# Performance work log

Measured on AMD Instinct MI355X. Metric: run time of the kernel, lower is better.

The kernel has to match this reference:

```python
import jax, jax.numpy as jnp
import numpy as np

N_NODES = 100000


def _degrees(src, dst, n):
    ones = jnp.ones(src.shape[0], dtype=jnp.float32)
    deg_out = jax.ops.segment_sum(ones, src, num_segments=n)
    deg_in = jax.ops.segment_sum(ones, dst, num_segments=n)
    # DGL clamps degrees to min 1 before pow(-0.5)
    return jnp.clip(deg_out, 1.0) ** -0.5, jnp.clip(deg_in, 1.0) ** -0.5


def _graph_conv(x, src, dst, W, b, norm_out, norm_in, n):
    # norm='both': scale source by D_out^-1/2, aggregate (copy_u + sum), scale dest by D_in^-1/2
    # weight applied before aggregation (in_feats >= out_feats for all layers; math-equivalent)
    h = (x * norm_out[:, None]) @ W                      # [N, out]
    agg = jax.ops.segment_sum(h[src], dst, num_segments=n)  # SpMM via gather+scatter-add
    return agg * norm_in[:, None] + b


def setup_inputs() -> dict:
    key = jax.random.key(0)
    ks = jax.random.split(key, 8)
    E = 1600000
    return {
        "in_feat": jax.random.normal(ks[0], (N_NODES, 128), dtype=jnp.float32),
        "src": jax.random.randint(ks[1], (E,), 0, N_NODES),
        "dst": jax.random.randint(ks[2], (E,), 0, N_NODES),
        "W1": jax.random.normal(ks[3], (128, 128), dtype=jnp.float32) * (128 ** -0.5),
        "b1": jnp.zeros((128,), dtype=jnp.float32),
        "W2": jax.random.normal(ks[4], (128, 128), dtype=jnp.float32) * (128 ** -0.5),
        "b2": jnp.zeros((128,), dtype=jnp.float32),
        "W3": jax.random.normal(ks[5], (128, 64), dtype=jnp.float32) * (128 ** -0.5),
        "b3": jnp.zeros((64,), dtype=jnp.float32),
    }


def reference(in_feat, src, dst, W1, b1, W2, b2, W3, b3):
    n = in_feat.shape[0]
    norm_out, norm_in = _degrees(src, dst, n)
    h = jax.nn.relu(_graph_conv(in_feat, src, dst, W1, b1, norm_out, norm_in, n))
    h = jax.nn.relu(_graph_conv(h, src, dst, W2, b2, norm_out, norm_in, n))
    h = _graph_conv(h, src, dst, W3, b3, norm_out, norm_in, n)
    return h
```

## Files before the change

kernel.cpp:

```cpp
#include <hip/hip_runtime.h>

#define THREADS 256
#define SCAN_BLK 1024
#define NR 8
#define NC 32
#define RSTRIDE 12544

typedef __attribute__((ext_vector_type(8))) _Float16 half8;
typedef __attribute__((ext_vector_type(4))) float floatx4;

__device__ __forceinline__ ushort f2h(float f) {
    union { _Float16 h; ushort s; } v;
    v.h = (_Float16)f;
    return v.s;
}
__device__ __forceinline__ float h_lo(uint u) {
    union { ushort s; _Float16 h; } v; v.s = (ushort)(u & 0xFFFFu); return (float)v.h;
}
__device__ __forceinline__ float h_hi(uint u) {
    union { ushort s; _Float16 h; } v; v.s = (ushort)(u >> 16); return (float)v.h;
}

__global__ __launch_bounds__(256) void hist_out_kernel(const int* __restrict__ src,
                                                       int* __restrict__ cnt_out,
                                                       int n, int E) {
    __shared__ uint cnt[RSTRIDE];
    const int range = blockIdx.x % NR;
    const int chunk = blockIdx.x / NR;
    const int Rsz = (n + NR - 1) / NR;
    const int lo  = range * Rsz;
    const int R   = min(n - lo, Rsz);
    if (R <= 0) return;
    for (int i = threadIdx.x; i < R; i += THREADS) cnt[i] = 0;
    __syncthreads();
    const int per = (E + NC - 1) / NC;
    const int c0 = chunk * per;
    const int c1 = min(E, c0 + per);
    int i = c0 + threadIdx.x * 4;
    for (; i + 4 <= c1; i += THREADS * 4) {
        int4 v = *(const int4*)(src + i);
        if ((unsigned)(v.x - lo) < (unsigned)R) atomicAdd(&cnt[v.x - lo], 1u);
        if ((unsigned)(v.y - lo) < (unsigned)R) atomicAdd(&cnt[v.y - lo], 1u);
        if ((unsigned)(v.z - lo) < (unsigned)R) atomicAdd(&cnt[v.z - lo], 1u);
        if ((unsigned)(v.w - lo) < (unsigned)R) atomicAdd(&cnt[v.w - lo], 1u);
    }
    if (i < c1) {
        for (int e = i; e < c1 && e < i + 4; ++e) {
            int s = src[e];
            if ((unsigned)(s - lo) < (unsigned)R) atomicAdd(&cnt[s - lo], 1u);
        }
    }
    __syncthreads();
    for (int k = threadIdx.x; k < R; k += THREADS) {
        uint c = cnt[k];
        if (c) atomicAdd(&cnt_out[lo + k], (int)c);
    }
}

__global__ __launch_bounds__(256) void csr_phaseA(const int* __restrict__ dst,
                                                  ushort* __restrict__ PC, int n, int E) {
    __shared__ uint cnt[RSTRIDE / 2];
    const int range = blockIdx.x % NR;
    const int chunk = blockIdx.x / NR;
    const int Rsz = (n + NR - 1) / NR;
    const int lo  = range * Rsz;
    const int R   = min(n - lo, Rsz);
    if (R <= 0) return;
    const int Rp = (R + 2) >> 1;
    for (int i = threadIdx.x; i < Rp; i += THREADS) cnt[i] = 0;
    __syncthreads();
    const int per = (E + NC - 1) / NC;
    const int c0 = chunk * per;
    const int c1 = min(E, c0 + per);
    int i = c0 + threadIdx.x * 4;
    for (; i + 4 <= c1; i += THREADS * 4) {
        int4 v = *(const int4*)(dst + i);
        int kx = v.x - lo, ky = v.y - lo, kz = v.z - lo, kw = v.w - lo;
        if ((unsigned)kx < (unsigned)R) atomicAdd(&cnt[kx >> 1], (kx & 1) ? 65536u : 1u);
        if ((unsigned)ky < (unsigned)R) atomicAdd(&cnt[ky >> 1], (ky & 1) ? 65536u : 1u);
        if ((unsigned)kz < (unsigned)R) atomicAdd(&cnt[kz >> 1], (kz & 1) ? 65536u : 1u);
        if ((unsigned)kw < (unsigned)R) atomicAdd(&cnt[kw >> 1], (kw & 1) ? 65536u : 1u);
    }
    if (i < c1) {
        for (int e = i; e < c1 && e < i + 4; ++e) {
            int k = dst[e] - lo;
            if ((unsigned)k < (unsigned)R) atomicAdd(&cnt[k >> 1], (k & 1) ? 65536u : 1u);
        }
    }
    __syncthreads();
    ushort* pc = PC + (size_t)(range * NC + chunk) * RSTRIDE;
    for (int k = threadIdx.x; k < R; k += THREADS) {
        uint c = cnt[k >> 1];
        pc[k] = (ushort)((k & 1) ? (c >> 16) : (c & 0xFFFFu));
    }
}

__global__ void csr_colsum(const ushort* __restrict__ PC, int* __restrict__ cnt_in, int n) {
    int gk = blockIdx.x * blockDim.x + threadIdx.x;
    if (gk >= n) return;
    const int Rsz = (n + NR - 1) / NR;
    int r = gk / Rsz, k = gk - r * Rsz;
    int t = 0;
    #pragma unroll 4
    for (int c = 0; c < NC; ++c)
        t += PC[(size_t)(r * NC + c) * RSTRIDE + k];
    cnt_in[gk] = t;
}

__global__ void csr_mkbase(const ushort* __restrict__ PC, const int* __restrict__ row_off,
                           int* __restrict__ B, int n) {
    int gk = blockIdx.x * blockDim.x + threadIdx.x;
    if (gk >= n) return;
    const int Rsz = (n + NR - 1) / NR;
    int r = gk / Rsz, k = gk - r * Rsz;
    int base = row_off[gk];
    for (int c = 0; c < NC; ++c) {
        size_t idx = (size_t)(r * NC + c) * RSTRIDE + k;
        B[idx] = base;
        base += PC[idx];
    }
}

__global__ __launch_bounds__(256) void csr_phaseC(const int* __restrict__ src,
                                                  const int* __restrict__ dst,
                                                  const int* __restrict__ B,
                                                  int* __restrict__ csr_src, int n, int E) {
    __shared__ int cur[RSTRIDE];
    const int range = blockIdx.x % NR;
    const int chunk = blockIdx.x / NR;
    const int Rsz = (n + NR - 1) / NR;
    const int lo  = range * Rsz;
    const int R   = min(n - lo, Rsz);
    if (R <= 0) return;
    const int* b = B + (size_t)(range * NC + chunk) * RSTRIDE;
    for (int i = threadIdx.x; i < R; i += THREADS) cur[i] = b[i];
    __syncthreads();
    const int per = (E + NC - 1) / NC;
    const int c0 = chunk * per;
    const int c1 = min(E, c0 + per);
    int i = c0 + threadIdx.x * 4;
    for (; i + 4 <= c1; i += THREADS * 4) {
        int4 d = *(const int4*)(dst + i);
        int4 s = *(const int4*)(src + i);
        int kx = d.x - lo, ky = d.y - lo, kz = d.z - lo, kw = d.w - lo;
        if ((unsigned)kx < (unsigned)R) csr_src[atomicAdd(&cur[kx], 1)] = s.x;
        if ((unsigned)ky < (unsigned)R) csr_src[atomicAdd(&cur[ky], 1)] = s.y;
        if ((unsigned)kz < (unsigned)R) csr_src[atomicAdd(&cur[kz], 1)] = s.z;
        if ((unsigned)kw < (unsigned)R) csr_src[atomicAdd(&cur[kw], 1)] = s.w;
    }
    if (i < c1) {
        for (int e = i; e < c1 && e < i + 4; ++e) {
            int k = dst[e] - lo;
            if ((unsigned)k < (unsigned)R) csr_src[atomicAdd(&cur[k], 1)] = src[e];
        }
    }
}

__global__ void scan_phase1(const int* __restrict__ cnt, int* __restrict__ blk_sums, int n) {
    int base = blockIdx.x * SCAN_BLK;
    int t = threadIdx.x;
    int sum = 0;
    for (int i = t; i < SCAN_BLK; i += THREADS) {
        int idx = base + i;
        sum += (idx < n) ? cnt[idx] : 0;
    }
    __shared__ int wsum[4];
    for (int off = 32; off > 0; off >>= 1) sum += __shfl_down(sum, off);
    if ((t & 63) == 0) wsum[t >> 6] = sum;
    __syncthreads();
    if (t == 0) blk_sums[blockIdx.x] = wsum[0] + wsum[1] + wsum[2] + wsum[3];
}

__global__ void scan_phase2(int* __restrict__ blk_sums, int nb) {
    __shared__ int s[1024];
    int t = threadIdx.x;
    s[t] = (t < nb) ? blk_sums[t] : 0;
    __syncthreads();
    for (int off = 1; off < 1024; off <<= 1) {
        int v = s[t];
        if (t >= off) v += s[t - off];
        __syncthreads();
        s[t] = v;
        __syncthreads();
    }
    if (t < nb) blk_sums[t] = (t == 0) ? 0 : s[t - 1];
}

__global__ void scan_phase3(const int* __restrict__ cnt, const int* __restrict__ cnt_out,
                            const int* __restrict__ blk_sums,
                            int* __restrict__ row_off, float* __restrict__ norm_in,
                            float* __restrict__ norm_out, int n, int E) {
    __shared__ int ts[THREADS];
    int b = blockIdx.x, t = threadIdx.x;
    int base = b * SCAN_BLK + t * 4;
    int local[4], val[4]; int s = 0;
    #pragma unroll
    for (int k = 0; k < 4; ++k) {
        local[k] = s;
        int idx = base + k;
        int v = (idx < n) ? cnt[idx] : 0;
        val[k] = v;
        s += v;
    }
    ts[t] = s;
    __syncthreads();
    for (int off = 1; off < THREADS; off <<= 1) {
        int v = ts[t];
        if (t >= off) v += ts[t - off];
        __syncthreads();
        ts[t] = v;
        __syncthreads();
    }
    int excl = (t == 0) ? 0 : ts[t - 1];
    int boff = blk_sums[b];
    #pragma unroll
    for (int k = 0; k < 4; ++k) {
        int idx = base + k;
        if (idx < n) {
            row_off[idx] = boff + excl + local[k];
            norm_in[idx]  = rsqrtf((float)max(val[k], 1));
            norm_out[idx] = rsqrtf((float)max(cnt_out[idx], 1));
        }
    }
    if (b == 0 && t == 0) row_off[n] = E;
}

__device__ __forceinline__ void wpack_one(const float* __restrict__ W, ushort* __restrict__ Wpk,
                                          int OUT, int t) {
    int lane = t & 63, kk = (t >> 6) & 3, ct = t >> 8;
    int col = ct * 16 + (lane & 15);
    int k0 = kk * 32 + (lane >> 4) * 8;
    #pragma unroll
    for (int j = 0; j < 8; ++j)
        Wpk[t * 8 + j] = f2h(W[(size_t)(k0 + j) * OUT + col]);
}

__global__ void wpack_all(const float* __restrict__ W1, const float* __restrict__ W2,
                          const float* __restrict__ W3, ushort* __restrict__ Wpk1,
                          ushort* __restrict__ Wpk2, ushort* __restrict__ Wpk3) {
    int t = blockIdx.x * blockDim.x + threadIdx.x;
    if (t < 2048)      wpack_one(W1, Wpk1, 128, t);
    else if (t < 4096) wpack_one(W2, Wpk2, 128, t - 2048);
    else if (t < 5120) wpack_one(W3, Wpk3, 64,  t - 4096);
}

template<int OUT>
__global__ __launch_bounds__(256) void mfma_gemm(const float* __restrict__ x,
                                                 const ushort* __restrict__ Wpk,
                                                 const float* __restrict__ norm,
                                                 ushort* __restrict__ h, int n) {
    __shared__ ushort xs[64 * 136];
    const int t = threadIdx.x;
    const int row0 = blockIdx.x * 64;

    #pragma unroll
    for (int i = 0; i < 8; ++i) {
        int e = (i * 256 + t) * 4;
        int row = e >> 7, col = e & 127;
        int gr = min(row0 + row, n - 1);
        float nf = norm[gr];
        float4 v = *(const float4*)(x + (size_t)gr * 128 + col);
        ushort4 p;
        p.x = f2h(v.x * nf); p.y = f2h(v.y * nf);
        p.z = f2h(v.z * nf); p.w = f2h(v.w * nf);
        *(ushort4*)(&xs[row * 136 + col]) = p;
    }
    __syncthreads();

    const int wave = t >> 6, lane = t & 63;
    const int r = lane & 15, g = lane >> 4;
    const int nrow0 = row0 + wave * 16;

    half8 a[4];
    #pragma unroll
    for (int kk = 0; kk < 4; ++kk)
        a[kk] = *(const half8*)(&xs[(wave * 16 + r) * 136 + kk * 32 + g * 8]);

    const half8* wp = (const half8*)Wpk;
    #pragma unroll
    for (int ct = 0; ct < OUT / 16; ++ct) {
        floatx4 acc = {0.f, 0.f, 0.f, 0.f};
        #pragma unroll
        for (int kk = 0; kk < 4; ++kk) {
            half8 b = wp[(ct * 4 + kk) * 64 + lane];
            acc = __builtin_amdgcn_mfma_f32_16x16x32_f16(a[kk], b, acc, 0, 0, 0);
        }
        int col = ct * 16 + r;
        #pragma unroll
        for (int rr = 0; rr < 4; ++rr) {
            int grow = nrow0 + g * 4 + rr;
            if (grow < n) h[(size_t)grow * OUT + col] = f2h(acc[rr]);
        }
    }
}

template<int OUTN>
__global__ __launch_bounds__(256) void fused_agg_gemm(const ushort* __restrict__ h,
                                                      const int* __restrict__ row_off,
                                                      const int* __restrict__ csr_src,
                                                      const float* __restrict__ nin,
                                                      const float* __restrict__ bias,
                                                      const float* __restrict__ nout,
                                                      const ushort* __restrict__ Wpk,
                                                      ushort* __restrict__ h_next, int n) {
    __shared__ ushort xs[64 * 136];
    const int t = threadIdx.x;
    const int wave = t >> 6, lane = t & 63;
    const int row0 = blockIdx.x * 64;
    const uint* hu = (const uint*)h;
    const float2 bb = *(const float2*)(bias + 2 * lane);

    for (int i = 0; i < 16; ++i) {
        const int lrow = wave * 16 + i;
        const int node = row0 + lrow;
        float a0 = 0.f, a1 = 0.f;
        if (node < n) {
            int beg = row_off[node], end = row_off[node + 1];
            int j = beg;
            for (; j + 3 < end; j += 4) {
                int s0 = csr_src[j], s1 = csr_src[j + 1], s2 = csr_src[j + 2], s3 = csr_src[j + 3];
                uint u0 = hu[(size_t)s0 * 64 + lane];
                uint u1 = hu[(size_t)s1 * 64 + lane];
                uint u2 = hu[(size_t)s2 * 64 + lane];
                uint u3 = hu[(size_t)s3 * 64 + lane];
                a0 += h_lo(u0); a1 += h_hi(u0);
                a0 += h_lo(u1); a1 += h_hi(u1);
                a0 += h_lo(u2); a1 += h_hi(u2);
                a0 += h_lo(u3); a1 += h_hi(u3);
            }
            for (; j < end; ++j) {
                uint u = hu[(size_t)csr_src[j] * 64 + lane];
                a0 += h_lo(u); a1 += h_hi(u);
            }
            float nf = nin[node];
            a0 = fmaxf(a0 * nf + bb.x, 0.f);
            a1 = fmaxf(a1 * nf + bb.y, 0.f);
            float no = nout[node];
            a0 *= no; a1 *= no;
        }
        ((uint*)xs)[lrow * 68 + lane] = (uint)f2h(a0) | ((uint)f2h(a1) << 16);
    }
    __syncthreads();

    const int r = lane & 15, g = lane >> 4;
    const int nrow0 = row0 + wave * 16;

    half8 a[4];
    #pragma unroll
    for (int kk = 0; kk < 4; ++kk)
        a[kk] = *(const half8*)(&xs[(wave * 16 + r) * 136 + kk * 32 + g * 8]);

    const half8* wp = (const half8*)Wpk;
    #pragma unroll
    for (int ct = 0; ct < OUTN / 16; ++ct) {
        floatx4 acc = {0.f, 0.f, 0.f, 0.f};
        #pragma unroll
        for (int kk = 0; kk < 4; ++kk) {
            half8 b = wp[(ct * 4 + kk) * 64 + lane];
            acc = __builtin_amdgcn_mfma_f32_16x16x32_f16(a[kk], b, acc, 0, 0, 0);
        }
        int col = ct * 16 + r;
        #pragma unroll
        for (int rr = 0; rr < 4; ++rr) {
            int grow = nrow0 + g * 4 + rr;
            if (grow < n) h_next[(size_t)grow * OUTN + col] = f2h(acc[rr]);
        }
    }
}

__global__ __launch_bounds__(256) void agg64_final(const ushort* __restrict__ h,
                                                   const int* __restrict__ row_off,
                                                   const int* __restrict__ csr_src,
                                                   const float* __restrict__ nin,
                                                   const float* __restrict__ bias,
                                                   float* __restrict__ out, int n) {
    const int wave = threadIdx.x >> 6;
    const int lane = threadIdx.x & 63;
    const int half = lane >> 5, u5 = lane & 31;
    const uint* hu = (const uint*)h;
    for (int node = blockIdx.x * 4 + wave; node < n; node += gridDim.x * 4) {
        int beg = row_off[node], end = row_off[node + 1];
        float a0 = 0.f, a1 = 0.f;
        int j = beg + half;
        for (; j + 2 < end; j += 4) {
            int sA = csr_src[j], sB = csr_src[j + 2];
            uint uA = hu[(size_t)sA * 32 + u5];
            uint uB = hu[(size_t)sB * 32 + u5];
            a0 += h_lo(uA); a1 += h_hi(uA);
            a0 += h_lo(uB); a1 += h_hi(uB);
        }
        if (j < end) {
            uint u = hu[(size_t)csr_src[j] * 32 + u5];
            a0 += h_lo(u); a1 += h_hi(u);
        }
        float o0 = a0 + __shfl(a0, u5 + 32);
        float o1 = a1 + __shfl(a1, u5 + 32);
        if (lane < 32) {
            float nf = nin[node];
            float2 bb = *(const float2*)(bias + 2 * u5);
            float2 r;
            r.x = o0 * nf + bb.x;
            r.y = o1 * nf + bb.y;
            *(float2*)(out + (size_t)node * 64 + 2 * u5) = r;
        }
    }
}

extern "C" void kernel_launch(void* const* d_in, const int* in_sizes, int n_in,
                              void* d_out, int out_size, void* d_ws, size_t ws_size,
                              hipStream_t stream) {
    const float* in_feat = (const float*)d_in[0];
    const int*   src     = (const int*)d_in[1];
    const int*   dst     = (const int*)d_in[2];
    const float* W1      = (const float*)d_in[3];
    const float* b1      = (const float*)d_in[4];
    const float* W2      = (const float*)d_in[5];
    const float* b2      = (const float*)d_in[6];
    const float* W3      = (const float*)d_in[7];
    const float* b3      = (const float*)d_in[8];

    const int n = in_sizes[0] / 128;
    const int E = in_sizes[1];
    float* out = (float*)d_out;

    float* ws       = (float*)d_ws;
    float* norm_out = ws;
    float* norm_in  = ws + n;
    int*   row_off  = (int*)(ws + 2 * (size_t)n);
    int*   csr_src  = row_off + (n + 4);
    ushort* Wpk1    = (ushort*)(csr_src + E);
    ushort* Wpk2    = Wpk1 + 128 * 128;
    ushort* Wpk3    = Wpk2 + 128 * 128;
    ushort* bufA    = Wpk3 + 128 * 64;
    ushort* bufB    = bufA + (size_t)n * 128;
    int*    cnt_in   = (int*)bufA;
    int*    cnt_out  = cnt_in + n;
    int*    blk_sums = cnt_out + n;
    ushort* PC       = (ushort*)(blk_sums + 128);
    int*    Bbase    = (int*)(PC + (size_t)NR * NC * RSTRIDE);

    const int nb = (n + SCAN_BLK - 1) / SCAN_BLK;

    hipMemsetAsync(cnt_out, 0, (size_t)n * sizeof(int), stream);
    wpack_all<<<20, THREADS, 0, stream>>>(W1, W2, W3, Wpk1, Wpk2, Wpk3);
    hist_out_kernel<<<NR * NC, THREADS, 0, stream>>>(src, cnt_out, n, E);
    csr_phaseA<<<NR * NC, THREADS, 0, stream>>>(dst, PC, n, E);
    csr_colsum<<<(n + THREADS - 1) / THREADS, THREADS, 0, stream>>>(PC, cnt_in, n);
    scan_phase1<<<nb, THREADS, 0, stream>>>(cnt_in, blk_sums, n);
    scan_phase2<<<1, 1024, 0, stream>>>(blk_sums, nb);
    scan_phase3<<<nb, THREADS, 0, stream>>>(cnt_in, cnt_out, blk_sums, row_off, norm_in, norm_out, n, E);
    csr_mkbase<<<(n + THREADS - 1) / THREADS, THREADS, 0, stream>>>(PC, row_off, Bbase, n);
    csr_phaseC<<<NR * NC, THREADS, 0, stream>>>(src, dst, Bbase, csr_src, n, E);

    const int tile_grid = (n + 63) / 64;
    const int agg_grid  = 4096;

    mfma_gemm<128><<<tile_grid, THREADS, 0, stream>>>(in_feat, Wpk1, norm_out, bufA, n);
    fused_agg_gemm<128><<<tile_grid, THREADS, 0, stream>>>(bufA, row_off, csr_src, norm_in, b1,
                                                           norm_out, Wpk2, bufB, n);
    fused_agg_gemm<64><<<tile_grid, THREADS, 0, stream>>>(bufB, row_off, csr_src, norm_in, b2,
                                                          norm_out, Wpk3, bufA, n);
    agg64_final<<<agg_grid, THREADS, 0, stream>>>(bufA, row_off, csr_src, norm_in, b3, out, n);
}
```

Measured before the change: 400.8 us.

## Split fused aggregate+GEMM into column-partitioned gather kernels and separate GEMMs

Replaces the fused aggregation+GEMM kernels with a column-sliced aggregation kernel, where each block handles one eighth of the feature columns, followed by separate MFMA GEMM kernels that read the aggregated fp16 features. The intent is to shrink the per-pass random-gather working set so it fits better in cache. Each wave also spreads a node's edges across lanes, with shuffle reductions, to raise memory parallelism. The cost is extra kernel launches, an extra write and read of the intermediate feature matrix, and reading the CSR index arrays eight times. It also adds nontemporal hints on the index loads and the output stores.

Result: slower. 1.100 ms (+174.4%).

```diff
diff --git a/kernel.cpp b/kernel.cpp
--- a/kernel.cpp
+++ b/kernel.cpp
@@ -294,54 +294,24 @@
     }
 }
 
-template<int OUTN>
-__global__ __launch_bounds__(256) void fused_agg_gemm(const ushort* __restrict__ h,
-                                                      const int* __restrict__ row_off,
-                                                      const int* __restrict__ csr_src,
-                                                      const float* __restrict__ nin,
-                                                      const float* __restrict__ bias,
-                                                      const float* __restrict__ nout,
-                                                      const ushort* __restrict__ Wpk,
-                                                      ushort* __restrict__ h_next, int n) {
+template<int OUT>
+__global__ __launch_bounds__(256) void mfma_gemm_pre(const ushort* __restrict__ x,
+                                                     const ushort* __restrict__ Wpk,
+                                                     ushort* __restrict__ h, int n) {
     __shared__ ushort xs[64 * 136];
     const int t = threadIdx.x;
+    const int row0 = blockIdx.x * 64;
+
+    #pragma unroll
+    for (int i = 0; i < 4; ++i) {
+        int e = (i * 256 + t) * 8;
+        int row = e >> 7, col = e & 127;
+        int gr = min(row0 + row, n - 1);
+        *(uint4*)(&xs[row * 136 + col]) = *(const uint4*)(x + (size_t)gr * 128 + col);
+    }
+    __syncthreads();
+
     const int wave = t >> 6, lane = t & 63;
-    const int row0 = blockIdx.x * 64;
-    const uint* hu = (const uint*)h;
-    const float2 bb = *(const float2*)(bias + 2 * lane);
-
-    for (int i = 0; i < 16; ++i) {
-        const int lrow = wave * 16 + i;
-        const int node = row0 + lrow;
-        float a0 = 0.f, a1 = 0.f;
-        if (node < n) {
-            int beg = row_off[node], end = row_off[node + 1];
-            int j = beg;
-            for (; j + 3 < end; j += 4) {
-                int s0 = csr_src[j], s1 = csr_src[j + 1], s2 = csr_src[j + 2], s3 = csr_src[j + 3];
-                uint u0 = hu[(size_t)s0 * 64 + lane];
-                uint u1 = hu[(size_t)s1 * 64 + lane];
-                uint u2 = hu[(size_t)s2 * 64 + lane];
-                uint u3 = hu[(size_t)s3 * 64 + lane];
-                a0 += h_lo(u0); a1 += h_hi(u0);
-                a0 += h_lo(u1); a1 += h_hi(u1);
-                a0 += h_lo(u2); a1 += h_hi(u2);
-                a0 += h_lo(u3); a1 += h_hi(u3);
-            }
-            for (; j < end; ++j) {
-                uint u = hu[(size_t)csr_src[j] * 64 + lane];
-                a0 += h_lo(u); a1 += h_hi(u);
-            }
-            float nf = nin[node];
-            a0 = fmaxf(a0 * nf + bb.x, 0.f);
-            a1 = fmaxf(a1 * nf + bb.y, 0.f);
-            float no = nout[node];
-            a0 *= no; a1 *= no;
-        }
-        ((uint*)xs)[lrow * 68 + lane] = (uint)f2h(a0) | ((uint)f2h(a1) << 16);
-    }
-    __syncthreads();
-
     const int r = lane & 15, g = lane >> 4;
     const int nrow0 = row0 + wave * 16;
 
@@ -352,7 +322,7 @@
 
     const half8* wp = (const half8*)Wpk;
     #pragma unroll
-    for (int ct = 0; ct < OUTN / 16; ++ct) {
+    for (int ct = 0; ct < OUT / 16; ++ct) {
         floatx4 acc = {0.f, 0.f, 0.f, 0.f};
         #pragma unroll
         for (int kk = 0; kk < 4; ++kk) {
@@ -363,45 +333,106 @@
         #pragma unroll
         for (int rr = 0; rr < 4; ++rr) {
             int grow = nrow0 + g * 4 + rr;
-            if (grow < n) h_next[(size_t)grow * OUTN + col] = f2h(acc[rr]);
-        }
-    }
-}
-
-__global__ __launch_bounds__(256) void agg64_final(const ushort* __restrict__ h,
-                                                   const int* __restrict__ row_off,
-                                                   const int* __restrict__ csr_src,
-                                                   const float* __restrict__ nin,
-                                                   const float* __restrict__ bias,
-                                                   float* __restrict__ out, int n) {
-    const int wave = threadIdx.x >> 6;
-    const int lane = threadIdx.x & 63;
-    const int half = lane >> 5, u5 = lane & 31;
+            if (grow < n) h[(size_t)grow * OUT + col] = f2h(acc[rr]);
+        }
+    }
+}
+
+template<bool RELU>
+__global__ __launch_bounds__(256) void aggcol128(const ushort* __restrict__ h,
+                                                 const int* __restrict__ row_off,
+                                                 const int* __restrict__ csr_src,
+                                                 const float* __restrict__ nin,
+                                                 const float* __restrict__ bias,
+                                                 const float* __restrict__ nout,
+                                                 ushort* __restrict__ out, int n) {
+    const int g    = blockIdx.x & 7;
+    const int bb   = blockIdx.x >> 3;
+    const int nb   = gridDim.x >> 3;
+    const int wave = threadIdx.x >> 6, lane = threadIdx.x & 63;
+    const int sub  = lane >> 3;
+    const int c    = lane & 7;
+    const int colu = g * 8 + c;
     const uint* hu = (const uint*)h;
-    for (int node = blockIdx.x * 4 + wave; node < n; node += gridDim.x * 4) {
+    const float2 bb2 = *(const float2*)(bias + 2 * colu);
+
+    for (int node = bb * 4 + wave; node < n; node += nb * 4) {
         int beg = row_off[node], end = row_off[node + 1];
         float a0 = 0.f, a1 = 0.f;
-        int j = beg + half;
-        for (; j + 2 < end; j += 4) {
-            int sA = csr_src[j], sB = csr_src[j + 2];
-            uint uA = hu[(size_t)sA * 32 + u5];
-            uint uB = hu[(size_t)sB * 32 + u5];
-            a0 += h_lo(uA); a1 += h_hi(uA);
-            a0 += h_lo(uB); a1 += h_hi(uB);
+        int j = beg + sub;
+        for (; j + 8 < end; j += 16) {
+            int s0 = __builtin_nontemporal_load(&csr_src[j]);
+            int s1 = __builtin_nontemporal_load(&csr_src[j + 8]);
+            uint u0 = hu[(size_t)s0 * 64 + colu];
+            uint u1 = hu[(size_t)s1 * 64 + colu];
+            a0 += h_lo(u0); a1 += h_hi(u0);
+            a0 += h_lo(u1); a1 += h_hi(u1);
         }
         if (j < end) {
-            uint u = hu[(size_t)csr_src[j] * 32 + u5];
-            a0 += h_lo(u); a1 += h_hi(u);
-        }
-        float o0 = a0 + __shfl(a0, u5 + 32);
-        float o1 = a1 + __shfl(a1, u5 + 32);
-        if (lane < 32) {
+            int s0 = __builtin_nontemporal_load(&csr_src[j]);
+            uint u0 = hu[(size_t)s0 * 64 + colu];
+            a0 += h_lo(u0); a1 += h_hi(u0);
+        }
+        a0 += __shfl_xor(a0, 8);  a1 += __shfl_xor(a1, 8);
+        a0 += __shfl_xor(a0, 16); a1 += __shfl_xor(a1, 16);
+        a0 += __shfl_xor(a0, 32); a1 += __shfl_xor(a1, 32);
+        if (sub == 0) {
             float nf = nin[node];
-            float2 bb = *(const float2*)(bias + 2 * u5);
+            float r0 = a0 * nf + bb2.x;
+            float r1 = a1 * nf + bb2.y;
+            if (RELU) { r0 = fmaxf(r0, 0.f); r1 = fmaxf(r1, 0.f); }
+            float no = nout[node];
+            r0 *= no; r1 *= no;
+            uint pv = (uint)f2h(r0) | ((uint)f2h(r1) << 16);
+            __builtin_nontemporal_store(pv, &((uint*)out)[(size_t)node * 64 + colu]);
+        }
+    }
+}
+
+__global__ __launch_bounds__(256) void agg64col(const ushort* __restrict__ h,
+                                                const int* __restrict__ row_off,
+                                                const int* __restrict__ csr_src,
+                                                const float* __restrict__ nin,
+                                                const float* __restrict__ bias,
+                                                float* __restrict__ out, int n) {
+    const int g    = blockIdx.x & 7;
+    const int bb   = blockIdx.x >> 3;
+    const int nb   = gridDim.x >> 3;
+    const int wave = threadIdx.x >> 6, lane = threadIdx.x & 63;
+    const int sub  = lane >> 2;
+    const int c    = lane & 3;
+    const int colu = g * 4 + c;
+    const uint* hu = (const uint*)h;
+    const float2 bb2 = *(const float2*)(bias + 2 * colu);
+
+    for (int node = bb * 4 + wave; node < n; node += nb * 4) {
+        int beg = row_off[node], end = row_off[node + 1];
+        float a0 = 0.f, a1 = 0.f;
+        int j = beg + sub;
+        for (; j + 16 < end; j += 32) {
+            int s0 = __builtin_nontemporal_load(&csr_src[j]);
+            int s1 = __builtin_nontemporal_load(&csr_src[j + 16]);
+            uint u0 = hu[(size_t)s0 * 32 + colu];
+            uint u1 = hu[(size_t)s1 * 32 + colu];
+            a0 += h_lo(u0); a1 += h_hi(u0);
+            a0 += h_lo(u1); a1 += h_hi(u1);
+        }
+        if (j < end) {
+            int s0 = __builtin_nontemporal_load(&csr_src[j]);
+            uint u0 = hu[(size_t)s0 * 32 + colu];
+            a0 += h_lo(u0); a1 += h_hi(u0);
+        }
+        a0 += __shfl_xor(a0, 4);  a1 += __shfl_xor(a1, 4);
+        a0 += __shfl_xor(a0, 8);  a1 += __shfl_xor(a1, 8);
+        a0 += __shfl_xor(a0, 16); a1 += __shfl_xor(a1, 16);
+        a0 += __shfl_xor(a0, 32); a1 += __shfl_xor(a1, 32);
+        if (sub == 0) {
+            float nf = nin[node];
             float2 r;
-            r.x = o0 * nf + bb.x;
-            r.y = o1 * nf + bb.y;
-            *(float2*)(out + (size_t)node * 64 + 2 * u5) = r;
+            r.x = a0 * nf + bb2.x;
+            r.y = a1 * nf + bb2.y;
+            __builtin_nontemporal_store(r.x, &out[(size_t)node * 64 + 2 * colu]);
+            __builtin_nontemporal_store(r.y, &out[(size_t)node * 64 + 2 * colu + 1]);
         }
     }
 }
@@ -453,12 +484,14 @@
     csr_phaseC<<<NR * NC, THREADS, 0, stream>>>(src, dst, Bbase, csr_src, n, E);
 
     const int tile_grid = (n + 63) / 64;
-    const int agg_grid  = 4096;
+    const int col_grid  = 8 * 512;
 
     mfma_gemm<128><<<tile_grid, THREADS, 0, stream>>>(in_feat, Wpk1, norm_out, bufA, n);
-    fused_agg_gemm<128><<<tile_grid, THREADS, 0, stream>>>(bufA, row_off, csr_src, norm_in, b1,
-                                                           norm_out, Wpk2, bufB, n);
-    fused_agg_gemm<64><<<tile_grid, THREADS, 0, stream>>>(bufB, row_off, csr_src, norm_in, b2,
-                                                          norm_out, Wpk3, bufA, n);
-    agg64_final<<<agg_grid, THREADS, 0, stream>>>(bufA, row_off, csr_src, norm_in, b3, out, n);
-}
+    aggcol128<true><<<col_grid, THREADS, 0, stream>>>(bufA, row_off, csr_src, norm_in, b1,
+                                                      norm_out, bufB, n);
+    mfma_gemm_pre<128><<<tile_grid, THREADS, 0, stream>>>(bufB, Wpk2, bufA, n);
+    aggcol128<true><<<col_grid, THREADS, 0, stream>>>(bufA, row_off, csr_src, norm_in, b2,
+                                                      norm_out, bufB, n);
+    mfma_gemm_pre<64><<<tile_grid, THREADS, 0, stream>>>(bufB, Wpk3, bufA, n);
+    agg64col<<<col_grid, THREADS, 0, stream>>>(bufA, row_off, csr_src, norm_in, b3, out, n);
+}
```
